# Performance work log

Measured on AMD Instinct MI355X. Metric: run time of the kernel, lower is better.

The kernel has to match this reference:

```python
import jax, jax.numpy as jnp
import numpy as np

N = 10000
E = 160000
F_IN = 2000
HEADS = 10
C1 = 128      # layer-1 per-head out channels
C2 = 128      # layer-2 per-head out channels (latent_dim)
NEG_SLOPE = 0.2
EPS = 1e-16


def gat_conv(x, W, att_src, att_dst, bias, src, dst, heads, out_ch, concat):
    """PyG-style GATConv (eval mode, self-loops already included in src/dst).
    x: [N, F_in]; W: [F_in, heads*out_ch]; att_*: [heads, out_ch]; bias: [out_dim].
    src/dst: [E'] edge endpoints (message flows src -> dst).
    """
    n = x.shape[0]
    h = (x @ W).reshape(n, heads, out_ch)              # [N, H, C]
    a_src = jnp.einsum('nhc,hc->nh', h, att_src)       # [N, H]
    a_dst = jnp.einsum('nhc,hc->nh', h, att_dst)       # [N, H]
    e = a_src[src] + a_dst[dst]                        # [E', H]
    e = jax.nn.leaky_relu(e, NEG_SLOPE)
    # segment softmax over incoming edges of each destination node
    m = jax.ops.segment_max(e, dst, num_segments=n)    # [N, H]
    ex = jnp.exp(e - m[dst])
    s = jax.ops.segment_sum(ex, dst, num_segments=n)   # [N, H]
    alpha = ex / (s[dst] + EPS)                        # [E', H]
    msg = h[src] * alpha[:, :, None]                   # [E', H, C]
    out = jax.ops.segment_sum(msg, dst, num_segments=n)  # [N, H, C]
    out = out.reshape(n, heads * out_ch) if concat else out.mean(axis=1)
    return out + bias


def setup_inputs() -> dict:
    key = jax.random.key(0)
    ks = jax.random.split(key, 10)
    glorot = lambda k, shape: jax.random.normal(k, shape, jnp.float32) * np.sqrt(2.0 / (shape[0] + shape[-1]))
    x = jax.random.normal(ks[0], (N, F_IN), jnp.float32)
    edge_index = jax.random.randint(ks[1], (2, E), 0, N, jnp.int64)
    W1 = glorot(ks[2], (F_IN, HEADS * C1))
    att_src1 = glorot(ks[3], (HEADS, C1))
    att_dst1 = glorot(ks[4], (HEADS, C1))
    b1 = jnp.zeros((HEADS * C1,), jnp.float32)
    W2 = glorot(ks[5], (HEADS * C1, HEADS * C2))
    att_src2 = glorot(ks[6], (HEADS, C2))
    att_dst2 = glorot(ks[7], (HEADS, C2))
    b2 = jnp.zeros((C2,), jnp.float32)
    return dict(x=x, edge_index=edge_index, W1=W1, att_src1=att_src1,
                att_dst1=att_dst1, b1=b1, W2=W2, att_src2=att_src2,
                att_dst2=att_dst2, b2=b2)


def reference(x, edge_index, W1, att_src1, att_dst1, b1, W2, att_src2, att_dst2, b2):
    n = x.shape[0]
    loops = jnp.arange(n, dtype=edge_index.dtype)
    src = jnp.concatenate([edge_index[0], loops])  # add self-loops (PyG default)
    dst = jnp.concatenate([edge_index[1], loops])
    h = jax.nn.relu(gat_conv(x, W1, att_src1, att_dst1, b1, src, dst, HEADS, C1, True))
    z = jax.nn.relu(gat_conv(h, W2, att_src2, att_dst2, b2, src, dst, HEADS, C2, False))
    return z
```

## Files before the change

### kernel.cpp

```cpp
#include <hip/hip_runtime.h>

typedef unsigned short u16;
typedef __attribute__((ext_vector_type(8))) short bf16x8;
typedef __attribute__((ext_vector_type(4))) float f32x4;
typedef __attribute__((ext_vector_type(4))) unsigned u32x4;

#define NN    10000
#define EE    160000
#define ET    170000
#define FIN   2000
#define MPAD  10112
#define K1PAD 2048
#define NH    1280
#define HEADS 10
#define NT    10
#define NWG   790

__device__ __forceinline__ u16 f32_to_bf16(float f) {
    unsigned u = __float_as_uint(f);
    unsigned r = (u + 0x7fffu + ((u >> 16) & 1u)) >> 16;
    return (u16)r;
}
__device__ __forceinline__ float bf16lo(unsigned pv) { return __uint_as_float(pv << 16); }
__device__ __forceinline__ float bf16hi(unsigned pv) { return __uint_as_float(pv & 0xffff0000u); }

__device__ __forceinline__ void gload16(const u16* g, u16* l) {
    __builtin_amdgcn_global_load_lds(
        (const __attribute__((address_space(1))) void*)g,
        (__attribute__((address_space(3))) void*)l, 16, 0, 0);
}

__global__ __launch_bounds__(256) void k_prep(const float* __restrict__ x,
                                              uint2* __restrict__ A1,
                                              const float* __restrict__ W1,
                                              u16* __restrict__ B1t) {
    __shared__ float tile[32][33];
    const int bid = blockIdx.x;
    const int t = threadIdx.x;
    if (bid < 2048) {
        const int total = MPAD * (K1PAD / 4);
        for (int idx = bid * 256 + t; idx < total; idx += 2048 * 256) {
            int r = idx >> 9;
            int c = (idx & 511) << 2;
            float4 v = make_float4(0.f, 0.f, 0.f, 0.f);
            if (r < NN && c < FIN) v = *(const float4*)(x + (size_t)r * FIN + c);
            uint2 p;
            p.x = (unsigned)f32_to_bf16(v.x) | ((unsigned)f32_to_bf16(v.y) << 16);
            p.y = (unsigned)f32_to_bf16(v.z) | ((unsigned)f32_to_bf16(v.w) << 16);
            A1[idx] = p;
        }
        return;
    }
    const int tx = t & 31, ty = t >> 5;
    int b = bid - 2048;
    int k0 = (b & 63) * 32, n0 = (b >> 6) * 32;
    #pragma unroll
    for (int i = 0; i < 32; i += 8) {
        int k = k0 + ty + i;
        tile[ty + i][tx] = (k < FIN) ? W1[(size_t)k * NH + n0 + tx] : 0.f;
    }
    __syncthreads();
    #pragma unroll
    for (int i = 0; i < 32; i += 8) {
        int n = n0 + ty + i, k = k0 + tx;
        B1t[(size_t)n * K1PAD + k] = f32_to_bf16(tile[tx][ty + i]);
    }
}

__global__ __launch_bounds__(256) void k_prepW2(const float* __restrict__ W2,
                                                u16* __restrict__ B2t) {
    __shared__ float tile[32][33];
    const int t = threadIdx.x;
    const int tx = t & 31, ty = t >> 5;
    int b = blockIdx.x;
    int k0 = (b % 40) * 32, n0 = (b / 40) * 32;
    #pragma unroll
    for (int i = 0; i < 32; i += 8)
        tile[ty + i][tx] = W2[(size_t)(k0 + ty + i) * NH + n0 + tx];
    __syncthreads();
    #pragma unroll
    for (int i = 0; i < 32; i += 8) {
        int n = n0 + ty + i, k = k0 + tx;
        B2t[(size_t)n * NH + k] = f32_to_bf16(tile[tx][ty + i]);
    }
}


template <bool AHM>
__global__ __launch_bounds__(512) void k_gemm(const u16* __restrict__ A,
                                              const u16* __restrict__ Bt,
                                              u16* __restrict__ Chm,
                                              const int Kpad, const int kTiles,
                                              const float* __restrict__ att_s,
                                              const float* __restrict__ att_d,
                                              float* __restrict__ a_srcp,
                                              float* __restrict__ a_dstp) {
    __shared__ __attribute__((aligned(16))) u16 S[32768];
    const int bid = blockIdx.x;
    const int xcd = bid & 7, idx = bid >> 3;
    const int q = NWG >> 3, r = NWG & 7;
    const int L = (xcd < r) ? (xcd * (q + 1) + idx)
                            : (r * (q + 1) + (xcd - r) * q + idx);
    const size_t m0 = (size_t)(L / NT) * 128, n0 = (size_t)(L % NT) * 128;
    const int h = (int)(n0 >> 7);

    const int t = threadIdx.x;
    const int lane = t & 63;
    const int wave = t >> 6;
    const int wr = wave >> 2, wc = wave & 3;

    f32x4 acc[4][2] = {};

    const int srow = t >> 3;
    const int klocal = (((t & 7) ^ ((t >> 3) & 7)) << 3);
    const u16* aRow = AHM ? (A + (m0 + srow) * 128 + klocal)
                          : (A + (m0 + srow) * (size_t)Kpad + klocal);
    const u16* bRow = Bt + (n0 + srow) * (size_t)Kpad + klocal;
    const size_t aStep = AHM ? (size_t)64 * 128 : (size_t)64 * Kpad;
    const size_t bStep = (size_t)64 * Kpad;

#define STAGE(kt_, bufb_) do {                                                   \
        char* db = (char*)S + (bufb_) + wave * 1024;                             \
        const u16* aP;                                                           \
        if (AHM) aP = aRow + (size_t)((kt_) >> 1) * (MPAD << 7) + ((kt_) & 1) * 64; \
        else     aP = aRow + (size_t)(kt_) * 64;                                 \
        const u16* bP = bRow + (size_t)(kt_) * 64;                               \
        gload16(aP,         (u16*)(db));                                         \
        gload16(aP + aStep, (u16*)(db + 8192));                                  \
        gload16(bP,         (u16*)(db + 16384));                                 \
        gload16(bP + bStep, (u16*)(db + 24576));                                 \
    } while (0)

    STAGE(0, 0);

    const int rl = lane & 15;
    const int kchunk = lane >> 4;
    const int xorv = (rl & 7) << 4;
    const int aBase0 = (wr * 64 + rl) * 128;
    const int bBase0 = (wc * 32 + rl) * 128;
    const char* Sb = (const char*)S;

    for (int kt = 0; kt < kTiles; ++kt) {
        asm volatile("s_waitcnt vmcnt(0)" ::: "memory");
        __builtin_amdgcn_s_barrier();
        if (kt + 1 < kTiles) STAGE(kt + 1, ((kt + 1) & 1) * 32768);
        const int bufo = (kt & 1) * 32768;
        #pragma unroll
        for (int ks = 0; ks < 2; ++ks) {
            const int px = (ks * 64 + kchunk * 16) ^ xorv;
            bf16x8 af[4], bfr[2];
            #pragma unroll
            for (int mf = 0; mf < 4; ++mf)
                af[mf] = *(const bf16x8*)(Sb + bufo + aBase0 + mf * 2048 + px);
            #pragma unroll
            for (int nf = 0; nf < 2; ++nf)
                bfr[nf] = *(const bf16x8*)(Sb + bufo + 16384 + bBase0 + nf * 2048 + px);
            #pragma unroll
            for (int mf = 0; mf < 4; ++mf)
                #pragma unroll
                for (int nf = 0; nf < 2; ++nf)
                    acc[mf][nf] = __builtin_amdgcn_mfma_f32_16x16x32_bf16(
                        af[mf], bfr[nf], acc[mf][nf], 0, 0, 0);
        }
    }
#undef STAGE

    float* red_s = (float*)S;
    float* red_d = red_s + 128;
    __syncthreads();
    if (t < 128) { red_s[t] = 0.f; red_d[t] = 0.f; }
    __syncthreads();

    const float as0 = att_s[h * 128 + wc * 32 + rl];
    const float as1 = att_s[h * 128 + wc * 32 + 16 + rl];
    const float ad0 = att_d[h * 128 + wc * 32 + rl];
    const float ad1 = att_d[h * 128 + wc * 32 + 16 + rl];
    #pragma unroll
    for (int mf = 0; mf < 4; ++mf)
        #pragma unroll
        for (int i = 0; i < 4; ++i) {
            float ps = acc[mf][0][i] * as0 + acc[mf][1][i] * as1;
            float pd = acc[mf][0][i] * ad0 + acc[mf][1][i] * ad1;
            #pragma unroll
            for (int o = 1; o < 16; o <<= 1) {
                ps += __shfl_xor(ps, o);
                pd += __shfl_xor(pd, o);
            }
            if (rl == 0) {
                int rloc = wr * 64 + mf * 16 + (lane >> 4) * 4 + i;
                atomicAdd(&red_s[rloc], ps);
                atomicAdd(&red_d[rloc], pd);
            }
        }
    __syncthreads();
    if (t < 128) {
        size_t nrow = m0 + t;
        if (nrow < NN) {
            a_srcp[nrow * HEADS + h] = red_s[t];
            a_dstp[nrow * HEADS + h] = red_d[t];
        }
    }

    u16* Cb = Chm + (size_t)h * (MPAD << 7);
    #pragma unroll
    for (int mf = 0; mf < 4; ++mf)
        #pragma unroll
        for (int i = 0; i < 4; ++i) {
            size_t row = m0 + wr * 64 + mf * 16 + (lane >> 4) * 4 + i;
            u16* crow = Cb + row * 128 + wc * 32 + rl;
            #pragma unroll
            for (int nf = 0; nf < 2; ++nf)
                crow[nf * 16] = f32_to_bf16(acc[mf][nf][i]);
        }
}

__global__ void k_count(const int* __restrict__ ei, int* __restrict__ deg) {
    int e = blockIdx.x * blockDim.x + threadIdx.x;
    if (e >= ET) return;
    int d = (e < EE) ? ei[EE + e] : (e - EE);
    atomicAdd(&deg[d], 1);
}

__global__ __launch_bounds__(256) void k_scan(const int* __restrict__ deg,
                                              int* __restrict__ off,
                                              int* __restrict__ cursor) {
    __shared__ int wt[4];
    const int t = threadIdx.x, lane = t & 63, w = t >> 6;
    const int lo = t * 40;
    const int hi = (lo + 40 < NN) ? lo + 40 : NN;
    int s = 0;
    for (int i = lo; i < hi; ++i) s += deg[i];
    int x = s;
    #pragma unroll
    for (int o = 1; o < 64; o <<= 1) { int y = __shfl_up(x, o); if (lane >= o) x += y; }
    if (lane == 63) wt[w] = x;
    __syncthreads();
    int wp = 0;
    for (int k = 0; k < w; ++k) wp += wt[k];
    int run = wp + x - s;
    for (int i = lo; i < hi; ++i) { off[i] = run; cursor[i] = run; run += deg[i]; }
    if (t == 255) off[NN] = wp + x;
}

__global__ void k_scatter(const int* __restrict__ ei, int* __restrict__ cursor,
                          int* __restrict__ csr_src) {
    int e = blockIdx.x * blockDim.x + threadIdx.x;
    if (e >= ET) return;
    int s = (e < EE) ? ei[e] : (e - EE);
    int d = (e < EE) ? ei[EE + e] : (e - EE);
    int pos = atomicAdd(&cursor[d], 1);
    csr_src[pos] = s;
}

template <int LAYER>
__global__ __launch_bounds__(256) void k_agg(const u16* __restrict__ Hhm,
                                             const float* __restrict__ a_src,
                                             const float* __restrict__ a_dst,
                                             const int* __restrict__ off,
                                             const int* __restrict__ csr,
                                             const float* __restrict__ bias,
                                             unsigned* __restrict__ outp) {
    const int bid = blockIdx.x;
    if (LAYER == 1 && bid >= 6256) {
        int idx = (bid - 6256) * 256 + threadIdx.x;
        int hh = idx / 7168, rr = idx - hh * 7168;
        int row = NN + (rr >> 6), dw = rr & 63;
        outp[((size_t)hh * MPAD + row) * 64 + dw] = 0u;
        return;
    }
    const int xcd = bid & 7, slot = bid >> 3;
    const int wv = threadIdx.x >> 6, lane = threadIdx.x & 63;
    const int u = slot * 4 + wv;
    if (u >= 3125) return;
    int h, qd;
    if (u < 2500) { h = xcd; qd = u; }
    else {
        int qg = xcd * 625 + (u - 2500);
        h = 8 + (qg >= 2500);
        qd = (qg >= 2500) ? qg - 2500 : qg;
    }
    const int g = lane >> 4, l = lane & 15;
    const int n = qd * 4 + g;
    const int beg = off[n], end = off[n + 1];
    const u16* Hh = Hhm + (size_t)h * (MPAD * 128);
    const float ad = a_dst[n * HEADS + h];

    float acc[8] = {};
    float den = 0.f;
    int i = beg;
    for (; i + 1 < end; i += 2) {
        const int s0 = csr[i], s1 = csr[i + 1];
        float e0 = a_src[s0 * HEADS + h] + ad; e0 = (e0 >= 0.f) ? e0 : 0.2f * e0;
        float e1 = a_src[s1 * HEADS + h] + ad; e1 = (e1 >= 0.f) ? e1 : 0.2f * e1;
        const float w0 = __expf(e0), w1 = __expf(e1);
        const u32x4 v0 = *(const u32x4*)(Hh + (size_t)s0 * 128 + l * 8);
        const u32x4 v1 = *(const u32x4*)(Hh + (size_t)s1 * 128 + l * 8);
        den += w0 + w1;
        #pragma unroll
        for (int j = 0; j < 4; ++j) {
            acc[2 * j]     = fmaf(bf16lo(v0[j]), w0, acc[2 * j]);
            acc[2 * j + 1] = fmaf(bf16hi(v0[j]), w0, acc[2 * j + 1]);
            acc[2 * j]     = fmaf(bf16lo(v1[j]), w1, acc[2 * j]);
            acc[2 * j + 1] = fmaf(bf16hi(v1[j]), w1, acc[2 * j + 1]);
        }
    }
    if (i < end) {
        const int s0 = csr[i];
        float e0 = a_src[s0 * HEADS + h] + ad; e0 = (e0 >= 0.f) ? e0 : 0.2f * e0;
        const float w0 = __expf(e0);
        const u32x4 v0 = *(const u32x4*)(Hh + (size_t)s0 * 128 + l * 8);
        den += w0;
        #pragma unroll
        for (int j = 0; j < 4; ++j) {
            acc[2 * j]     = fmaf(bf16lo(v0[j]), w0, acc[2 * j]);
            acc[2 * j + 1] = fmaf(bf16hi(v0[j]), w0, acc[2 * j + 1]);
        }
    }
    const float si = 1.f / (den + 1e-16f);

    u32x4 pk;
    if (LAYER == 1) {
        const int c = h * 128 + l * 8;
        #pragma unroll
        for (int j = 0; j < 4; ++j) {
            float v0 = fmaxf(fmaf(acc[2 * j],     si, bias[c + 2 * j]),     0.f);
            float v1 = fmaxf(fmaf(acc[2 * j + 1], si, bias[c + 2 * j + 1]), 0.f);
            pk[j] = (unsigned)f32_to_bf16(v0) | ((unsigned)f32_to_bf16(v1) << 16);
        }
    } else {
        #pragma unroll
        for (int j = 0; j < 4; ++j) {
            pk[j] = (unsigned)f32_to_bf16(acc[2 * j] * si)
                  | ((unsigned)f32_to_bf16(acc[2 * j + 1] * si) << 16);
        }
    }
    *(u32x4*)(outp + (size_t)h * (MPAD * 64) + (size_t)n * 64 + l * 4) = pk;
}

__global__ __launch_bounds__(256) void k_final(const unsigned* __restrict__ Z,
                                               const float* __restrict__ b2,
                                               float* __restrict__ out) {
    int t = blockIdx.x * 256 + threadIdx.x;
    if (t >= NN * 64) return;
    int n = t >> 6, d = t & 63;
    float s0 = 0.f, s1 = 0.f;
    #pragma unroll
    for (int h = 0; h < HEADS; ++h) {
        unsigned pv = Z[(size_t)h * (MPAD * 64) + (size_t)n * 64 + d];
        s0 += bf16lo(pv);
        s1 += bf16hi(pv);
    }
    float2 z;
    z.x = fmaxf(fmaf(s0, 0.1f, b2[2 * d]),     0.f);
    z.y = fmaxf(fmaf(s1, 0.1f, b2[2 * d + 1]), 0.f);
    *(float2*)(out + (size_t)n * 128 + 2 * d) = z;
}

extern "C" void kernel_launch(void* const* d_in, const int* in_sizes, int n_in,
                              void* d_out, int out_size, void* d_ws, size_t ws_size,
                              hipStream_t stream) {
    const float* x   = (const float*)d_in[0];
    const int*   ei  = (const int*)  d_in[1];
    const float* W1  = (const float*)d_in[2];
    const float* as1 = (const float*)d_in[3];
    const float* ad1 = (const float*)d_in[4];
    const float* b1  = (const float*)d_in[5];
    const float* W2  = (const float*)d_in[6];
    const float* as2 = (const float*)d_in[7];
    const float* ad2 = (const float*)d_in[8];
    const float* b2  = (const float*)d_in[9];

    char* ws = (char*)d_ws;
    const size_t A1_OFF  = 0;
    const size_t A2_OFF  = 0;
    const size_t B2T_OFF = (size_t)MPAD * NH * 2;
    const size_t H_OFF   = (size_t)MPAD * K1PAD * 2;
    const size_t B1T_OFF = H_OFF + (size_t)MPAD * NH * 2;
    size_t o = B1T_OFF + (size_t)NH * K1PAD * 2;
    const size_t AS_OFF  = o; o += 400128;
    const size_t AD_OFF  = o; o += 400128;
    const size_t DEG_OFF = o; o += 40064;
    const size_t OFF_OFF = o; o += 40064;
    const size_t CUR_OFF = o; o += 40064;
    const size_t CSR_OFF = o; o += 680064;
    if (ws_size < o) return;

    u16*      A1   = (u16*)(ws + A1_OFF);
    unsigned* A2   = (unsigned*)(ws + A2_OFF);
    u16*      B2t  = (u16*)(ws + B2T_OFF);
    u16*      H    = (u16*)(ws + H_OFF);
    u16*      B1t  = (u16*)(ws + B1T_OFF);
    float*    aS   = (float*)(ws + AS_OFF);
    float*    aD   = (float*)(ws + AD_OFF);
    int*      deg  = (int*)(ws + DEG_OFF);
    int*      offp = (int*)(ws + OFF_OFF);
    int*      cur  = (int*)(ws + CUR_OFF);
    int*      csr  = (int*)(ws + CSR_OFF);

    hipMemsetAsync(deg, 0, NN * sizeof(int), stream);
    k_count<<<(ET + 255) / 256, 256, 0, stream>>>(ei, deg);
    k_scan<<<1, 256, 0, stream>>>(deg, offp, cur);
    k_scatter<<<(ET + 255) / 256, 256, 0, stream>>>(ei, cur, csr);

    k_prep<<<4608, 256, 0, stream>>>(x, (uint2*)A1, W1, B1t);

    k_gemm<false><<<NWG, 512, 0, stream>>>(A1, B1t, H, K1PAD, K1PAD / 64,
                                           as1, ad1, aS, aD);
    k_prepW2<<<1600, 256, 0, stream>>>(W2, B2t);
    k_agg<1><<<6536, 256, 0, stream>>>(H, aS, aD, offp, csr, b1, A2);

    k_gemm<true><<<NWG, 512, 0, stream>>>((u16*)A2, B2t, H, NH, NH / 64,
                                          as2, ad2, aS, aD);
    k_agg<2><<<6256, 256, 0, stream>>>(H, aS, aD, offp, csr, b2, A2);
    k_final<<<(NN * 64 + 255) / 256, 256, 0, stream>>>(A2, b2, (float*)d_out);
}
```

Measured before the change: 291.4 us.

## Move attention-logit reduction out of GEMM epilogue into separate kernel with head-major layout

Drops the fused attention dot-product epilogue (shuffles, LDS atomics, extra barriers) from both GEMMs. A new k_attn kernel computes a_src/a_dst from the bf16 H output, and stores them head-major so each aggregation wave reads contiguous per-head logits. This adds two kernel launches and an extra read of H, and the logits now come from bf16-rounded H instead of fp32 accumulators, a small accuracy change.

```diff
diff --git a/kernel.cpp b/kernel.cpp
--- a/kernel.cpp
+++ b/kernel.cpp
@@ -90,11 +90,7 @@
 __global__ __launch_bounds__(512) void k_gemm(const u16* __restrict__ A,
                                               const u16* __restrict__ Bt,
                                               u16* __restrict__ Chm,
-                                              const int Kpad, const int kTiles,
-                                              const float* __restrict__ att_s,
-                                              const float* __restrict__ att_d,
-                                              float* __restrict__ a_srcp,
-                                              float* __restrict__ a_dstp) {
+                                              const int Kpad, const int kTiles) {
     __shared__ __attribute__((aligned(16))) u16 S[32768];
     const int bid = blockIdx.x;
     const int xcd = bid & 7, idx = bid >> 3;
@@ -102,7 +98,6 @@
     const int L = (xcd < r) ? (xcd * (q + 1) + idx)
                             : (r * (q + 1) + (xcd - r) * q + idx);
     const size_t m0 = (size_t)(L / NT) * 128, n0 = (size_t)(L % NT) * 128;
-    const int h = (int)(n0 >> 7);
 
     const int t = threadIdx.x;
     const int lane = t & 63;
@@ -165,43 +160,7 @@
     }
 #undef STAGE
 
-    float* red_s = (float*)S;
-    float* red_d = red_s + 128;
-    __syncthreads();
-    if (t < 128) { red_s[t] = 0.f; red_d[t] = 0.f; }
-    __syncthreads();
-
-    const float as0 = att_s[h * 128 + wc * 32 + rl];
-    const float as1 = att_s[h * 128 + wc * 32 + 16 + rl];
-    const float ad0 = att_d[h * 128 + wc * 32 + rl];
-    const float ad1 = att_d[h * 128 + wc * 32 + 16 + rl];
-    #pragma unroll
-    for (int mf = 0; mf < 4; ++mf)
-        #pragma unroll
-        for (int i = 0; i < 4; ++i) {
-            float ps = acc[mf][0][i] * as0 + acc[mf][1][i] * as1;
-            float pd = acc[mf][0][i] * ad0 + acc[mf][1][i] * ad1;
-            #pragma unroll
-            for (int o = 1; o < 16; o <<= 1) {
-                ps += __shfl_xor(ps, o);
-                pd += __shfl_xor(pd, o);
-            }
-            if (rl == 0) {
-                int rloc = wr * 64 + mf * 16 + (lane >> 4) * 4 + i;
-                atomicAdd(&red_s[rloc], ps);
-                atomicAdd(&red_d[rloc], pd);
-            }
-        }
-    __syncthreads();
-    if (t < 128) {
-        size_t nrow = m0 + t;
-        if (nrow < NN) {
-            a_srcp[nrow * HEADS + h] = red_s[t];
-            a_dstp[nrow * HEADS + h] = red_d[t];
-        }
-    }
-
-    u16* Cb = Chm + (size_t)h * (MPAD << 7);
+    u16* Cb = Chm + (size_t)(n0 >> 7) * (MPAD << 7);
     #pragma unroll
     for (int mf = 0; mf < 4; ++mf)
         #pragma unroll
@@ -212,6 +171,28 @@
             for (int nf = 0; nf < 2; ++nf)
                 crow[nf * 16] = f32_to_bf16(acc[mf][nf][i]);
         }
+}
+
+__global__ __launch_bounds__(256) void k_attn(const u16* __restrict__ Hhm,
+                                              const float* __restrict__ att_s,
+                                              const float* __restrict__ att_d,
+                                              float* __restrict__ a_src,
+                                              float* __restrict__ a_dst) {
+    const int lane = threadIdx.x & 63;
+    const int n = blockIdx.x * 4 + (threadIdx.x >> 6);
+    if (n >= NN) return;
+    const unsigned* Hd = (const unsigned*)Hhm;
+    #pragma unroll
+    for (int h = 0; h < HEADS; ++h) {
+        unsigned pv = Hd[((size_t)h * MPAD + n) * 64 + lane];
+        float v0 = bf16lo(pv), v1 = bf16hi(pv);
+        int c = h * 128 + lane * 2;
+        float s = v0 * att_s[c] + v1 * att_s[c + 1];
+        float d = v0 * att_d[c] + v1 * att_d[c + 1];
+        #pragma unroll
+        for (int o = 32; o; o >>= 1) { s += __shfl_xor(s, o); d += __shfl_xor(d, o); }
+        if (lane == 0) { a_src[h * NN + n] = s; a_dst[h * NN + n] = d; }
+    }
 }
 
 __global__ void k_count(const int* __restrict__ ei, int* __restrict__ deg) {
@@ -283,15 +264,16 @@
     const int n = qd * 4 + g;
     const int beg = off[n], end = off[n + 1];
     const u16* Hh = Hhm + (size_t)h * (MPAD * 128);
-    const float ad = a_dst[n * HEADS + h];
+    const float* asl = a_src + (size_t)h * NN;
+    const float ad = a_dst[(size_t)h * NN + n];
 
     float acc[8] = {};
     float den = 0.f;
     int i = beg;
     for (; i + 1 < end; i += 2) {
         const int s0 = csr[i], s1 = csr[i + 1];
-        float e0 = a_src[s0 * HEADS + h] + ad; e0 = (e0 >= 0.f) ? e0 : 0.2f * e0;
-        float e1 = a_src[s1 * HEADS + h] + ad; e1 = (e1 >= 0.f) ? e1 : 0.2f * e1;
+        float e0 = asl[s0] + ad; e0 = (e0 >= 0.f) ? e0 : 0.2f * e0;
+        float e1 = asl[s1] + ad; e1 = (e1 >= 0.f) ? e1 : 0.2f * e1;
         const float w0 = __expf(e0), w1 = __expf(e1);
         const u32x4 v0 = *(const u32x4*)(Hh + (size_t)s0 * 128 + l * 8);
         const u32x4 v1 = *(const u32x4*)(Hh + (size_t)s1 * 128 + l * 8);
@@ -306,7 +288,7 @@
     }
     if (i < end) {
         const int s0 = csr[i];
-        float e0 = a_src[s0 * HEADS + h] + ad; e0 = (e0 >= 0.f) ? e0 : 0.2f * e0;
+        float e0 = asl[s0] + ad; e0 = (e0 >= 0.f) ? e0 : 0.2f * e0;
         const float w0 = __expf(e0);
         const u32x4 v0 = *(const u32x4*)(Hh + (size_t)s0 * 128 + l * 8);
         den += w0;
@@ -404,13 +386,13 @@
 
     k_prep<<<4608, 256, 0, stream>>>(x, (uint2*)A1, W1, B1t);
 
-    k_gemm<false><<<NWG, 512, 0, stream>>>(A1, B1t, H, K1PAD, K1PAD / 64,
-                                           as1, ad1, aS, aD);
+    k_gemm<false><<<NWG, 512, 0, stream>>>(A1, B1t, H, K1PAD, K1PAD / 64);
     k_prepW2<<<1600, 256, 0, stream>>>(W2, B2t);
+    k_attn<<<2500, 256, 0, stream>>>(H, as1, ad1, aS, aD);
     k_agg<1><<<6536, 256, 0, stream>>>(H, aS, aD, offp, csr, b1, A2);
 
-    k_gemm<true><<<NWG, 512, 0, stream>>>((u16*)A2, B2t, H, NH, NH / 64,
-                                          as2, ad2, aS, aD);
+    k_gemm<true><<<NWG, 512, 0, stream>>>((u16*)A2, B2t, H, NH, NH / 64);
+    k_attn<<<2500, 256, 0, stream>>>(H, as2, ad2, aS, aD);
     k_agg<2><<<6256, 256, 0, stream>>>(H, aS, aD, offp, csr, b2, A2);
     k_final<<<(NN * 64 + 255) / 256, 256, 0, stream>>>(A2, b2, (float*)d_out);
 }
```

After: 290.9 us. About the same (-0.2%).
